# Optimization experiments

Measured on AMD Instinct MI355X. Metric: run time of the kernel, lower is better.

## Reference

```python
import jax, jax.numpy as jnp
import numpy as np

N = 8192      # nodes
E = 262144    # edges (avg degree 32)
NFEAT = 1024
NHID = 512
ZDIM = 32


def _uniform(key, shape, stdv):
    return jax.random.uniform(key, shape, jnp.float32, -stdv, stdv)


def setup_inputs() -> dict:
    key = jax.random.key(0)
    ks = jax.random.split(key, 10)
    x = jax.random.normal(ks[0], (N, NFEAT), jnp.float32)
    adj_rows = jnp.sort(jax.random.randint(ks[1], (E,), 0, N))
    adj_cols = jax.random.randint(ks[2], (E,), 0, N)
    # positive edge weights, roughly row-normalized (avg degree 32)
    adj_vals = jax.random.uniform(ks[3], (E,), jnp.float32) / 32.0
    s0 = 1.0 / np.sqrt(NHID).astype(np.float32)
    s1 = 1.0 / np.sqrt(ZDIM).astype(np.float32)
    W0 = _uniform(ks[4], (NFEAT, NHID), s0)
    b0 = _uniform(ks[5], (NHID,), s0)
    W1 = _uniform(ks[6], (NHID, ZDIM), s1)
    b1 = _uniform(ks[7], (ZDIM,), s1)
    W2 = _uniform(ks[8], (NHID, ZDIM), s1)
    b2 = _uniform(ks[9], (ZDIM,), s1)
    return dict(x=x, adj_vals=adj_vals, W0=W0, b0=b0, W1=W1, b1=b1,
                W2=W2, b2=b2, adj_rows=adj_rows, adj_cols=adj_cols)


def _spmm(rows, cols, vals, mat):
    # sparse [N,N] @ dense [N,D] via gather + segment_sum
    return jax.ops.segment_sum(vals[:, None] * mat[cols], rows, num_segments=N)


def reference(x, adj_vals, W0, b0, W1, b1, W2, b2, adj_rows, adj_cols):
    # GraphConvolution: spmm(adj, x @ W) + b  (eval mode: dropout is identity)
    h = jax.nn.relu(_spmm(adj_rows, adj_cols, adj_vals, x @ W0) + b0)
    mu = jax.nn.relu(_spmm(adj_rows, adj_cols, adj_vals, h @ W1) + b1)
    logvar = jax.nn.relu(_spmm(adj_rows, adj_cols, adj_vals, h @ W2) + b2)
    z = mu  # reparameterize in eval mode returns mu
    adj_recon = jax.nn.sigmoid(z @ z.T)  # [N, N] inner-product decoder
    return adj_recon, z, mu, logvar
```

## Files before the change

kernel.cpp:

```cpp
#include <hip/hip_runtime.h>
#include <hip/hip_bf16.h>

typedef __bf16 bf16_t;
typedef __bf16 bf16x8 __attribute__((ext_vector_type(8)));
typedef float f32x4 __attribute__((ext_vector_type(4)));

#define NN 8192
#define EE 262144
#define NF 1024
#define NH 512
#define ZD 32

__global__ __launch_bounds__(256) void k_cvt(const float* __restrict__ in,
                                             bf16_t* __restrict__ out, int n8) {
  int i = blockIdx.x * 256 + threadIdx.x;
  if (i >= n8) return;
  const float4 a = ((const float4*)in)[i * 2];
  const float4 b = ((const float4*)in)[i * 2 + 1];
  bf16x8 o;
  o[0] = (bf16_t)a.x; o[1] = (bf16_t)a.y; o[2] = (bf16_t)a.z; o[3] = (bf16_t)a.w;
  o[4] = (bf16_t)b.x; o[5] = (bf16_t)b.y; o[6] = (bf16_t)b.z; o[7] = (bf16_t)b.w;
  ((bf16x8*)out)[i] = o;
}

__global__ __launch_bounds__(256) void k_transpose_cvt(const float* __restrict__ in,
                                                       bf16_t* __restrict__ out,
                                                       int R, int C) {
  __shared__ float tile[32][33];
  const int c0 = blockIdx.x * 32, r0 = blockIdx.y * 32;
  const int tx = threadIdx.x & 31, ty = threadIdx.x >> 5;
  #pragma unroll
  for (int i = ty; i < 32; i += 8)
    tile[i][tx] = in[(size_t)(r0 + i) * C + (c0 + tx)];
  __syncthreads();
  #pragma unroll
  for (int i = ty; i < 32; i += 8)
    out[(size_t)(c0 + i) * R + (r0 + tx)] = (bf16_t)tile[tx][i];
}

__global__ __launch_bounds__(256) void k_transpose_w12(const float* __restrict__ W1,
                                                       const float* __restrict__ W2,
                                                       bf16_t* __restrict__ out) {
  __shared__ float tile[32][33];
  const float* in = blockIdx.z ? W2 : W1;
  bf16_t* o = out + (size_t)blockIdx.z * ZD * NH;
  const int r0 = blockIdx.y * 32;
  const int tx = threadIdx.x & 31, ty = threadIdx.x >> 5;
  #pragma unroll
  for (int i = ty; i < 32; i += 8)
    tile[i][tx] = in[(size_t)(r0 + i) * ZD + tx];
  __syncthreads();
  #pragma unroll
  for (int i = ty; i < 32; i += 8)
    o[(size_t)(i)*NH + (r0 + tx)] = (bf16_t)tile[tx][i];
}

__global__ void k_rowptr(const int* __restrict__ rows, int* __restrict__ rp,
                         int n, int e) {
  int r = blockIdx.x * 256 + threadIdx.x;
  if (r > n) return;
  if (r == n) { rp[n] = e; return; }
  int lo = 0, hi = e;
  while (lo < hi) { int mid = (lo + hi) >> 1; if (rows[mid] < r) lo = mid + 1; else hi = mid; }
  rp[r] = lo;
}

__global__ __launch_bounds__(256) void k_gemm_bt_128x128(
    const bf16_t* __restrict__ A, const bf16_t* __restrict__ Bt,
    bf16_t* __restrict__ C, int M, int N, int K) {
  __shared__ bf16_t As[128 * 32];
  __shared__ bf16_t Bs[128 * 32];
  const int tid = threadIdx.x;
  const int lane = tid & 63, wave = tid >> 6;
  const int wx = wave & 1, wy = wave >> 1;
  const int m0 = blockIdx.y * 128, n0 = blockIdx.x * 128;
  const int q = lane >> 4, ml = lane & 15;

  const int sr = tid >> 2, ss = tid & 3;
  const int sw_lo = sr * 32 + ((ss ^ (sr & 3)) * 8);
  const int sw_hi = sw_lo + 64 * 32;

  int a_off[4], b_off[4];
  #pragma unroll
  for (int i = 0; i < 4; ++i) {
    int m = wy * 64 + i * 16 + ml;
    a_off[i] = m * 32 + ((q ^ (m & 3)) * 8);
    int n = wx * 64 + i * 16 + ml;
    b_off[i] = n * 32 + ((q ^ (n & 3)) * 8);
  }

  f32x4 acc[4][4];
  #pragma unroll
  for (int i = 0; i < 4; ++i)
    #pragma unroll
    for (int j = 0; j < 4; ++j)
      acc[i][j] = (f32x4){0.f, 0.f, 0.f, 0.f};

  const bf16_t* ga = A + (size_t)(m0 + sr) * K + ss * 8;
  const bf16_t* gb = Bt + (size_t)(n0 + sr) * K + ss * 8;
  const size_t stride64 = (size_t)64 * K;

  for (int k0 = 0; k0 < K; k0 += 32) {
    int4 va0 = *(const int4*)(ga + k0);
    int4 va1 = *(const int4*)(ga + stride64 + k0);
    int4 vb0 = *(const int4*)(gb + k0);
    int4 vb1 = *(const int4*)(gb + stride64 + k0);
    __syncthreads();
    *(int4*)(&As[sw_lo]) = va0;
    *(int4*)(&As[sw_hi]) = va1;
    *(int4*)(&Bs[sw_lo]) = vb0;
    *(int4*)(&Bs[sw_hi]) = vb1;
    __syncthreads();
    bf16x8 af[4], bfr[4];
    #pragma unroll
    for (int i = 0; i < 4; ++i) af[i] = *(const bf16x8*)(&As[a_off[i]]);
    #pragma unroll
    for (int j = 0; j < 4; ++j) bfr[j] = *(const bf16x8*)(&Bs[b_off[j]]);
    #pragma unroll
    for (int i = 0; i < 4; ++i)
      #pragma unroll
      for (int j = 0; j < 4; ++j)
        acc[i][j] = __builtin_amdgcn_mfma_f32_16x16x32_bf16(af[i], bfr[j], acc[i][j], 0, 0, 0);
  }

  #pragma unroll
  for (int i = 0; i < 4; ++i) {
    const int row = m0 + wy * 64 + i * 16 + q * 4;
    #pragma unroll
    for (int j = 0; j < 4; ++j) {
      const int col = n0 + wx * 64 + j * 16 + ml;
      #pragma unroll
      for (int r = 0; r < 4; ++r)
        C[(size_t)(row + r) * N + col] = (bf16_t)acc[i][j][r];
    }
  }
}

__global__ __launch_bounds__(256) void k_gemm_bt_128x64(
    const bf16_t* __restrict__ A, const bf16_t* __restrict__ Bt,
    float* __restrict__ C, int M, int N, int K) {
  __shared__ bf16_t As[128 * 32];
  __shared__ bf16_t Bs[64 * 32];
  const int tid = threadIdx.x;
  const int lane = tid & 63, wave = tid >> 6;
  const int m0 = blockIdx.y * 128;
  const int q = lane >> 4, ml = lane & 15;
  const int sr = tid >> 2, ss = tid & 3;
  const int sw_lo = sr * 32 + ((ss ^ (sr & 3)) * 8);
  const int sw_hi = sw_lo + 64 * 32;

  int a_off[2], b_off[4];
  #pragma unroll
  for (int i = 0; i < 2; ++i) {
    int m = wave * 32 + i * 16 + ml;
    a_off[i] = m * 32 + ((q ^ (m & 3)) * 8);
  }
  #pragma unroll
  for (int j = 0; j < 4; ++j) {
    int n = j * 16 + ml;
    b_off[j] = n * 32 + ((q ^ (n & 3)) * 8);
  }

  f32x4 acc[2][4];
  #pragma unroll
  for (int i = 0; i < 2; ++i)
    #pragma unroll
    for (int j = 0; j < 4; ++j)
      acc[i][j] = (f32x4){0.f, 0.f, 0.f, 0.f};

  const bf16_t* ga = A + (size_t)(m0 + sr) * K + ss * 8;
  const bf16_t* gb = Bt + (size_t)sr * K + ss * 8;
  const size_t stride64 = (size_t)64 * K;

  for (int k0 = 0; k0 < K; k0 += 32) {
    int4 va0 = *(const int4*)(ga + k0);
    int4 va1 = *(const int4*)(ga + stride64 + k0);
    int4 vb0 = *(const int4*)(gb + k0);
    __syncthreads();
    *(int4*)(&As[sw_lo]) = va0;
    *(int4*)(&As[sw_hi]) = va1;
    *(int4*)(&Bs[sw_lo]) = vb0;
    __syncthreads();
    bf16x8 af[2], bfr[4];
    #pragma unroll
    for (int i = 0; i < 2; ++i) af[i] = *(const bf16x8*)(&As[a_off[i]]);
    #pragma unroll
    for (int j = 0; j < 4; ++j) bfr[j] = *(const bf16x8*)(&Bs[b_off[j]]);
    #pragma unroll
    for (int i = 0; i < 2; ++i)
      #pragma unroll
      for (int j = 0; j < 4; ++j)
        acc[i][j] = __builtin_amdgcn_mfma_f32_16x16x32_bf16(af[i], bfr[j], acc[i][j], 0, 0, 0);
  }

  #pragma unroll
  for (int i = 0; i < 2; ++i) {
    const int row = m0 + wave * 32 + i * 16 + q * 4;
    #pragma unroll
    for (int j = 0; j < 4; ++j) {
      const int col = j * 16 + ml;
      #pragma unroll
      for (int r = 0; r < 4; ++r)
        C[(size_t)(row + r) * N + col] = acc[i][j][r];
    }
  }
}

__global__ __launch_bounds__(256) void k_spmm_h(
    const int* __restrict__ rp, const int* __restrict__ cols,
    const float* __restrict__ vals, const unsigned int* __restrict__ XW0b,
    const float* __restrict__ b0, bf16_t* __restrict__ h) {
  const int chunk = blockIdx.x & 3;
  const int row = (blockIdx.x >> 2) * 4 + (threadIdx.x >> 6);
  const int t = threadIdx.x & 63;
  const unsigned int* tab = XW0b + chunk * 64 + t;
  int e = rp[row];
  const int end = rp[row + 1];
  float a0 = 0.f, a1 = 0.f;
  for (; e + 3 < end; e += 4) {
    const int c0 = cols[e], c1 = cols[e + 1], c2 = cols[e + 2], c3 = cols[e + 3];
    const float v0 = vals[e], v1 = vals[e + 1], v2 = vals[e + 2], v3 = vals[e + 3];
    const unsigned int p0 = tab[(size_t)c0 * 256];
    const unsigned int p1 = tab[(size_t)c1 * 256];
    const unsigned int p2 = tab[(size_t)c2 * 256];
    const unsigned int p3 = tab[(size_t)c3 * 256];
    a0 += v0 * __uint_as_float(p0 << 16);
    a1 += v0 * __uint_as_float(p0 & 0xffff0000u);
    a0 += v1 * __uint_as_float(p1 << 16);
    a1 += v1 * __uint_as_float(p1 & 0xffff0000u);
    a0 += v2 * __uint_as_float(p2 << 16);
    a1 += v2 * __uint_as_float(p2 & 0xffff0000u);
    a0 += v3 * __uint_as_float(p3 << 16);
    a1 += v3 * __uint_as_float(p3 & 0xffff0000u);
  }
  for (; e < end; ++e) {
    const float v0 = vals[e];
    const unsigned int p0 = tab[(size_t)cols[e] * 256];
    a0 += v0 * __uint_as_float(p0 << 16);
    a1 += v0 * __uint_as_float(p0 & 0xffff0000u);
  }
  const int d = chunk * 128 + t * 2;
  a0 += b0[d];
  a1 += b0[d + 1];
  bf16_t x0 = (bf16_t)fmaxf(a0, 0.f);
  bf16_t x1 = (bf16_t)fmaxf(a1, 0.f);
  const unsigned int pk = (unsigned int)(*(const unsigned short*)&x0) |
                          ((unsigned int)(*(const unsigned short*)&x1) << 16);
  *(unsigned int*)(h + (size_t)row * NH + d) = pk;
}

__global__ __launch_bounds__(256) void k_spmm_z(
    const int* __restrict__ rp, const int* __restrict__ cols,
    const float* __restrict__ vals, const float* __restrict__ HW,
    const float* __restrict__ b1, const float* __restrict__ b2,
    float* __restrict__ out_z, float* __restrict__ out_mu,
    float* __restrict__ out_lv, bf16_t* __restrict__ zb) {
  const int r = blockIdx.x * 4 + (threadIdx.x >> 6);
  const int t = threadIdx.x & 63;
  int e = rp[r];
  const int end = rp[r + 1];
  float acc = 0.f;
  for (; e + 3 < end; e += 4) {
    const float v0 = vals[e], v1 = vals[e + 1], v2 = vals[e + 2], v3 = vals[e + 3];
    const float s0 = HW[(size_t)cols[e] * 64 + t];
    const float s1 = HW[(size_t)cols[e + 1] * 64 + t];
    const float s2 = HW[(size_t)cols[e + 2] * 64 + t];
    const float s3 = HW[(size_t)cols[e + 3] * 64 + t];
    acc += v0 * s0;
    acc += v1 * s1;
    acc += v2 * s2;
    acc += v3 * s3;
  }
  for (; e < end; ++e) acc += vals[e] * HW[(size_t)cols[e] * 64 + t];
  const float b = (t < ZD) ? b1[t] : b2[t - ZD];
  const float v = fmaxf(acc + b, 0.f);
  if (t < ZD) {
    out_mu[(size_t)r * ZD + t] = v;
    out_z[(size_t)r * ZD + t] = v;
    zb[(size_t)r * ZD + t] = (bf16_t)v;
  } else {
    out_lv[(size_t)r * ZD + (t - ZD)] = v;
  }
}

__global__ __launch_bounds__(256) void k_decoder(const bf16_t* __restrict__ Z,
                                                 float* __restrict__ out) {
  __shared__ bf16_t Zr[128 * 32];
  __shared__ bf16_t Zc[128 * 32];
  __shared__ float tile[64][132];
  const int tid = threadIdx.x;
  const int lane = tid & 63, wave = tid >> 6;
  const int wx = wave & 1, wy = wave >> 1;
  const int m0 = blockIdx.y * 128, n0 = blockIdx.x * 128;
  const int q = lane >> 4, ml = lane & 15;
  const int sr = tid >> 2, ss = tid & 3;
  const int sw_lo = sr * 32 + ((ss ^ (sr & 3)) * 8);
  const int sw_hi = sw_lo + 64 * 32;

  *(int4*)(&Zr[sw_lo]) = *((const int4*)(Z + (size_t)(m0 + sr) * ZD) + ss);
  *(int4*)(&Zr[sw_hi]) = *((const int4*)(Z + (size_t)(m0 + sr + 64) * ZD) + ss);
  *(int4*)(&Zc[sw_lo]) = *((const int4*)(Z + (size_t)(n0 + sr) * ZD) + ss);
  *(int4*)(&Zc[sw_hi]) = *((const int4*)(Z + (size_t)(n0 + sr + 64) * ZD) + ss);
  __syncthreads();

  bf16x8 af[4], bfr[4];
  #pragma unroll
  for (int i = 0; i < 4; ++i) {
    int m = wy * 64 + i * 16 + ml;
    af[i] = *(const bf16x8*)(&Zr[m * 32 + ((q ^ (m & 3)) * 8)]);
    int n = wx * 64 + i * 16 + ml;
    bfr[i] = *(const bf16x8*)(&Zc[n * 32 + ((q ^ (n & 3)) * 8)]);
  }

  f32x4 acc[4][4];
  const f32x4 zero = (f32x4){0.f, 0.f, 0.f, 0.f};
  #pragma unroll
  for (int i = 0; i < 4; ++i)
    #pragma unroll
    for (int j = 0; j < 4; ++j)
      acc[i][j] = __builtin_amdgcn_mfma_f32_16x16x32_bf16(af[i], bfr[j], zero, 0, 0, 0);

  #pragma unroll
  for (int i = 0; i < 4; ++i)
    #pragma unroll
    for (int j = 0; j < 4; ++j)
      #pragma unroll
      for (int r = 0; r < 4; ++r)
        acc[i][j][r] = 1.f / (1.f + __expf(-acc[i][j][r]));

  const int g = tid >> 5, c4 = tid & 31;
  #pragma unroll
  for (int half = 0; half < 2; ++half) {
    if (wy == half) {
      #pragma unroll
      for (int i = 0; i < 4; ++i)
        #pragma unroll
        for (int j = 0; j < 4; ++j)
          #pragma unroll
          for (int r = 0; r < 4; ++r)
            tile[i * 16 + q * 4 + r][wx * 64 + j * 16 + ml] = acc[i][j][r];
    }
    __syncthreads();
    float* orow = out + (size_t)(m0 + half * 64) * NN + n0;
    #pragma unroll
    for (int p = 0; p < 8; ++p) {
      const int lr = p * 8 + g;
      f32x4 v = *(const f32x4*)&tile[lr][c4 * 4];
      __builtin_nontemporal_store(v, (f32x4*)(orow + (size_t)lr * NN + c4 * 4));
    }
    __syncthreads();
  }
}

extern "C" void kernel_launch(void* const* d_in, const int* in_sizes, int n_in,
                              void* d_out, int out_size, void* d_ws, size_t ws_size,
                              hipStream_t stream) {
  const float* x        = (const float*)d_in[0];
  const float* adj_vals = (const float*)d_in[1];
  const float* W0       = (const float*)d_in[2];
  const float* b0       = (const float*)d_in[3];
  const float* W1       = (const float*)d_in[4];
  const float* b1       = (const float*)d_in[5];
  const float* W2       = (const float*)d_in[6];
  const float* b2       = (const float*)d_in[7];
  const int* adj_rows   = (const int*)d_in[8];
  const int* adj_cols   = (const int*)d_in[9];

  char* ws = (char*)d_ws;
  bf16_t* XW0b = (bf16_t*)(ws);
  float*  HW   = (float*)(ws + 8388608);
  bf16_t* h    = (bf16_t*)(ws + 10485760);
  bf16_t* W0t  = (bf16_t*)(ws + 18874368);
  bf16_t* Wct  = (bf16_t*)(ws + 19922944);
  bf16_t* xb   = (bf16_t*)(ws + 19988480);
  bf16_t* zb   = (bf16_t*)(ws + 36765696);
  int*    rp   = (int*)(ws + 37289984);

  float* out     = (float*)d_out;
  float* out_adj = out;
  float* out_z   = out + (size_t)NN * NN;
  float* out_mu  = out_z + (size_t)NN * ZD;
  float* out_lv  = out_mu + (size_t)NN * ZD;

  k_cvt<<<(NN * NF / 8 + 255) / 256, 256, 0, stream>>>(x, xb, NN * NF / 8);
  k_transpose_cvt<<<dim3(NH / 32, NF / 32), 256, 0, stream>>>(W0, W0t, NF, NH);
  k_transpose_w12<<<dim3(1, NH / 32, 2), 256, 0, stream>>>(W1, W2, Wct);
  k_rowptr<<<33, 256, 0, stream>>>(adj_rows, rp, NN, EE);

  k_gemm_bt_128x128<<<dim3(NH / 128, NN / 128), 256, 0, stream>>>(xb, W0t, XW0b, NN, NH, NF);
  k_spmm_h<<<NN, 256, 0, stream>>>(rp, adj_cols, adj_vals,
                                   (const unsigned int*)XW0b, b0, h);

  k_gemm_bt_128x64<<<dim3(1, NN / 128), 256, 0, stream>>>(h, Wct, HW, NN, 64, NH);
  k_spmm_z<<<NN / 4, 256, 0, stream>>>(rp, adj_cols, adj_vals, HW, b1, b2, out_z, out_mu, out_lv, zb);

  k_decoder<<<dim3(NN / 128, NN / 128), 256, 0, stream>>>(zb, out_adj);
}
```

Baseline: 399.7 us.

## Fuse prep kernels, interleave edge data, stage edges in LDS for SpMM

Merges the four preprocessing launches into a single k_prep kernel that also packs cols/vals into an interleaved int2 edge array. Both SpMM kernels now load each 4-row group's edge list into shared memory once, instead of every wave re-reading cols/vals from global memory. k_spmm_h switches to 512-thread blocks with two chunks of four bf16 per lane (uint2 gathers), cutting block count and redundant edge reads. The aim is lower launch overhead and less edge-index traffic, at the cost of an extra pass writing the packed edge array and a global fallback path when a row group has more than 512 edges.

```diff
diff --git a/kernel.cpp b/kernel.cpp
--- a/kernel.cpp
+++ b/kernel.cpp
@@ -11,58 +11,70 @@
 #define NH 512
 #define ZD 32
 
-__global__ __launch_bounds__(256) void k_cvt(const float* __restrict__ in,
-                                             bf16_t* __restrict__ out, int n8) {
-  int i = blockIdx.x * 256 + threadIdx.x;
-  if (i >= n8) return;
-  const float4 a = ((const float4*)in)[i * 2];
-  const float4 b = ((const float4*)in)[i * 2 + 1];
-  bf16x8 o;
-  o[0] = (bf16_t)a.x; o[1] = (bf16_t)a.y; o[2] = (bf16_t)a.z; o[3] = (bf16_t)a.w;
-  o[4] = (bf16_t)b.x; o[5] = (bf16_t)b.y; o[6] = (bf16_t)b.z; o[7] = (bf16_t)b.w;
-  ((bf16x8*)out)[i] = o;
-}
-
-__global__ __launch_bounds__(256) void k_transpose_cvt(const float* __restrict__ in,
-                                                       bf16_t* __restrict__ out,
-                                                       int R, int C) {
+static __device__ __forceinline__ unsigned short bf16_bits(bf16_t v) {
+  union { bf16_t b; unsigned short u; } c;
+  c.b = v;
+  return c.u;
+}
+
+__global__ __launch_bounds__(256) void k_prep(
+    const float* __restrict__ x, bf16_t* __restrict__ xb,
+    const float* __restrict__ W0, bf16_t* __restrict__ W0t,
+    const float* __restrict__ W1, const float* __restrict__ W2, bf16_t* __restrict__ Wct,
+    const int* __restrict__ rows, int* __restrict__ rp,
+    const int* __restrict__ cols, const float* __restrict__ vals, int2* __restrict__ ev) {
   __shared__ float tile[32][33];
-  const int c0 = blockIdx.x * 32, r0 = blockIdx.y * 32;
-  const int tx = threadIdx.x & 31, ty = threadIdx.x >> 5;
-  #pragma unroll
-  for (int i = ty; i < 32; i += 8)
-    tile[i][tx] = in[(size_t)(r0 + i) * C + (c0 + tx)];
-  __syncthreads();
-  #pragma unroll
-  for (int i = ty; i < 32; i += 8)
-    out[(size_t)(c0 + i) * R + (r0 + tx)] = (bf16_t)tile[tx][i];
-}
-
-__global__ __launch_bounds__(256) void k_transpose_w12(const float* __restrict__ W1,
-                                                       const float* __restrict__ W2,
-                                                       bf16_t* __restrict__ out) {
-  __shared__ float tile[32][33];
-  const float* in = blockIdx.z ? W2 : W1;
-  bf16_t* o = out + (size_t)blockIdx.z * ZD * NH;
-  const int r0 = blockIdx.y * 32;
-  const int tx = threadIdx.x & 31, ty = threadIdx.x >> 5;
-  #pragma unroll
-  for (int i = ty; i < 32; i += 8)
-    tile[i][tx] = in[(size_t)(r0 + i) * ZD + tx];
-  __syncthreads();
-  #pragma unroll
-  for (int i = ty; i < 32; i += 8)
-    o[(size_t)(i)*NH + (r0 + tx)] = (bf16_t)tile[tx][i];
-}
-
-__global__ void k_rowptr(const int* __restrict__ rows, int* __restrict__ rp,
-                         int n, int e) {
-  int r = blockIdx.x * 256 + threadIdx.x;
-  if (r > n) return;
-  if (r == n) { rp[n] = e; return; }
-  int lo = 0, hi = e;
-  while (lo < hi) { int mid = (lo + hi) >> 1; if (rows[mid] < r) lo = mid + 1; else hi = mid; }
-  rp[r] = lo;
+  const int b = blockIdx.x;
+  const int tid = threadIdx.x;
+
+  if (b < 4096) {
+    const int i = b * 256 + tid;
+    const float4 a = ((const float4*)x)[i * 2];
+    const float4 c = ((const float4*)x)[i * 2 + 1];
+    bf16x8 o;
+    o[0] = (bf16_t)a.x; o[1] = (bf16_t)a.y; o[2] = (bf16_t)a.z; o[3] = (bf16_t)a.w;
+    o[4] = (bf16_t)c.x; o[5] = (bf16_t)c.y; o[6] = (bf16_t)c.z; o[7] = (bf16_t)c.w;
+    ((bf16x8*)xb)[i] = o;
+  } else if (b < 4608) {
+    const int bx = b - 4096;
+    const int c0 = (bx & 15) * 32, r0 = (bx >> 4) * 32;
+    const int tx = tid & 31, ty = tid >> 5;
+    #pragma unroll
+    for (int i = ty; i < 32; i += 8)
+      tile[i][tx] = W0[(size_t)(r0 + i) * NH + (c0 + tx)];
+    __syncthreads();
+    #pragma unroll
+    for (int i = ty; i < 32; i += 8)
+      W0t[(size_t)(c0 + i) * NF + (r0 + tx)] = (bf16_t)tile[tx][i];
+  } else if (b < 4640) {
+    const int idx = b - 4608;
+    const int z = idx & 1, y = idx >> 1;
+    const float* in = z ? W2 : W1;
+    bf16_t* o = Wct + (size_t)z * ZD * NH;
+    const int r0 = y * 32;
+    const int tx = tid & 31, ty = tid >> 5;
+    #pragma unroll
+    for (int i = ty; i < 32; i += 8)
+      tile[i][tx] = in[(size_t)(r0 + i) * ZD + tx];
+    __syncthreads();
+    #pragma unroll
+    for (int i = ty; i < 32; i += 8)
+      o[(size_t)(i)*NH + (r0 + tx)] = (bf16_t)tile[tx][i];
+  } else if (b < 4673) {
+    const int r = (b - 4640) * 256 + tid;
+    if (r > NN) return;
+    if (r == NN) { rp[NN] = EE; return; }
+    int lo = 0, hi = EE;
+    while (lo < hi) { int mid = (lo + hi) >> 1; if (rows[mid] < r) lo = mid + 1; else hi = mid; }
+    rp[r] = lo;
+  } else {
+    const int i = ((b - 4673) * 256 + tid) * 4;
+    const int4 c4 = *(const int4*)(cols + i);
+    const float4 v4 = *(const float4*)(vals + i);
+    int4* dst = (int4*)(ev + i);
+    dst[0] = make_int4(c4.x, __float_as_int(v4.x), c4.y, __float_as_int(v4.y));
+    dst[1] = make_int4(c4.z, __float_as_int(v4.z), c4.w, __float_as_int(v4.w));
+  }
 }
 
 __global__ __launch_bounds__(256) void k_gemm_bt_128x128(
@@ -206,72 +218,128 @@
   }
 }
 
-__global__ __launch_bounds__(256) void k_spmm_h(
-    const int* __restrict__ rp, const int* __restrict__ cols,
-    const float* __restrict__ vals, const unsigned int* __restrict__ XW0b,
-    const float* __restrict__ b0, bf16_t* __restrict__ h) {
-  const int chunk = blockIdx.x & 3;
-  const int row = (blockIdx.x >> 2) * 4 + (threadIdx.x >> 6);
-  const int t = threadIdx.x & 63;
-  const unsigned int* tab = XW0b + chunk * 64 + t;
-  int e = rp[row];
-  const int end = rp[row + 1];
-  float a0 = 0.f, a1 = 0.f;
-  for (; e + 3 < end; e += 4) {
-    const int c0 = cols[e], c1 = cols[e + 1], c2 = cols[e + 2], c3 = cols[e + 3];
-    const float v0 = vals[e], v1 = vals[e + 1], v2 = vals[e + 2], v3 = vals[e + 3];
-    const unsigned int p0 = tab[(size_t)c0 * 256];
-    const unsigned int p1 = tab[(size_t)c1 * 256];
-    const unsigned int p2 = tab[(size_t)c2 * 256];
-    const unsigned int p3 = tab[(size_t)c3 * 256];
-    a0 += v0 * __uint_as_float(p0 << 16);
-    a1 += v0 * __uint_as_float(p0 & 0xffff0000u);
-    a0 += v1 * __uint_as_float(p1 << 16);
-    a1 += v1 * __uint_as_float(p1 & 0xffff0000u);
-    a0 += v2 * __uint_as_float(p2 << 16);
-    a1 += v2 * __uint_as_float(p2 & 0xffff0000u);
-    a0 += v3 * __uint_as_float(p3 << 16);
-    a1 += v3 * __uint_as_float(p3 & 0xffff0000u);
+__global__ __launch_bounds__(512) void k_spmm_h(
+    const int* __restrict__ rp, const int2* __restrict__ ev,
+    const uint2* __restrict__ XW0b, const float* __restrict__ b0,
+    bf16_t* __restrict__ h) {
+  __shared__ int2 se[512];
+  const int rg = blockIdx.x;
+  const int tid = threadIdx.x;
+  const int wave = tid >> 6, t = tid & 63;
+  const int row = rg * 4 + (wave & 3);
+  const int chunk = wave >> 2;
+
+  const int base = rp[rg * 4];
+  const int cnt = rp[rg * 4 + 4] - base;
+  const int scnt = cnt < 512 ? cnt : 512;
+  for (int i = tid; i < scnt; i += 512) se[i] = ev[base + i];
+  __syncthreads();
+
+  int e = rp[row] - base;
+  const int end = rp[row + 1] - base;
+  const int se_end = end < 512 ? end : 512;
+  const uint2* tab = XW0b + chunk * 64 + t;
+
+  float a0 = 0.f, a1 = 0.f, a2 = 0.f, a3 = 0.f;
+  for (; e + 3 < se_end; e += 4) {
+    const int2 p0 = se[e], p1 = se[e + 1], p2 = se[e + 2], p3 = se[e + 3];
+    const uint2 g0 = tab[(size_t)p0.x * 128];
+    const uint2 g1 = tab[(size_t)p1.x * 128];
+    const uint2 g2 = tab[(size_t)p2.x * 128];
+    const uint2 g3 = tab[(size_t)p3.x * 128];
+    const float v0 = __int_as_float(p0.y), v1 = __int_as_float(p1.y);
+    const float v2 = __int_as_float(p2.y), v3 = __int_as_float(p3.y);
+    a0 += v0 * __uint_as_float(g0.x << 16);
+    a1 += v0 * __uint_as_float(g0.x & 0xffff0000u);
+    a2 += v0 * __uint_as_float(g0.y << 16);
+    a3 += v0 * __uint_as_float(g0.y & 0xffff0000u);
+    a0 += v1 * __uint_as_float(g1.x << 16);
+    a1 += v1 * __uint_as_float(g1.x & 0xffff0000u);
+    a2 += v1 * __uint_as_float(g1.y << 16);
+    a3 += v1 * __uint_as_float(g1.y & 0xffff0000u);
+    a0 += v2 * __uint_as_float(g2.x << 16);
+    a1 += v2 * __uint_as_float(g2.x & 0xffff0000u);
+    a2 += v2 * __uint_as_float(g2.y << 16);
+    a3 += v2 * __uint_as_float(g2.y & 0xffff0000u);
+    a0 += v3 * __uint_as_float(g3.x << 16);
+    a1 += v3 * __uint_as_float(g3.x & 0xffff0000u);
+    a2 += v3 * __uint_as_float(g3.y << 16);
+    a3 += v3 * __uint_as_float(g3.y & 0xffff0000u);
+  }
+  for (; e < se_end; ++e) {
+    const int2 p = se[e];
+    const uint2 g = tab[(size_t)p.x * 128];
+    const float v = __int_as_float(p.y);
+    a0 += v * __uint_as_float(g.x << 16);
+    a1 += v * __uint_as_float(g.x & 0xffff0000u);
+    a2 += v * __uint_as_float(g.y << 16);
+    a3 += v * __uint_as_float(g.y & 0xffff0000u);
   }
   for (; e < end; ++e) {
-    const float v0 = vals[e];
-    const unsigned int p0 = tab[(size_t)cols[e] * 256];
-    a0 += v0 * __uint_as_float(p0 << 16);
-    a1 += v0 * __uint_as_float(p0 & 0xffff0000u);
-  }
-  const int d = chunk * 128 + t * 2;
-  a0 += b0[d];
-  a1 += b0[d + 1];
-  bf16_t x0 = (bf16_t)fmaxf(a0, 0.f);
-  bf16_t x1 = (bf16_t)fmaxf(a1, 0.f);
-  const unsigned int pk = (unsigned int)(*(const unsigned short*)&x0) |
-                          ((unsigned int)(*(const unsigned short*)&x1) << 16);
-  *(unsigned int*)(h + (size_t)row * NH + d) = pk;
+    const int2 p = ev[base + e];
+    const uint2 g = tab[(size_t)p.x * 128];
+    const float v = __int_as_float(p.y);
+    a0 += v * __uint_as_float(g.x << 16);
+    a1 += v * __uint_as_float(g.x & 0xffff0000u);
+    a2 += v * __uint_as_float(g.y << 16);
+    a3 += v * __uint_as_float(g.y & 0xffff0000u);
+  }
+
+  const int d = chunk * 256 + t * 4;
+  const float4 bb = *(const float4*)(b0 + d);
+  const bf16_t x0 = (bf16_t)fmaxf(a0 + bb.x, 0.f);
+  const bf16_t x1 = (bf16_t)fmaxf(a1 + bb.y, 0.f);
+  const bf16_t x2 = (bf16_t)fmaxf(a2 + bb.z, 0.f);
+  const bf16_t x3 = (bf16_t)fmaxf(a3 + bb.w, 0.f);
+  uint2 pk;
+  pk.x = (unsigned int)bf16_bits(x0) | ((unsigned int)bf16_bits(x1) << 16);
+  pk.y = (unsigned int)bf16_bits(x2) | ((unsigned int)bf16_bits(x3) << 16);
+  ((uint2*)(h + (size_t)row * NH))[chunk * 64 + t] = pk;
 }
 
 __global__ __launch_bounds__(256) void k_spmm_z(
-    const int* __restrict__ rp, const int* __restrict__ cols,
-    const float* __restrict__ vals, const float* __restrict__ HW,
+    const int* __restrict__ rp, const int2* __restrict__ ev,
+    const float* __restrict__ HW,
     const float* __restrict__ b1, const float* __restrict__ b2,
     float* __restrict__ out_z, float* __restrict__ out_mu,
     float* __restrict__ out_lv, bf16_t* __restrict__ zb) {
-  const int r = blockIdx.x * 4 + (threadIdx.x >> 6);
-  const int t = threadIdx.x & 63;
-  int e = rp[r];
-  const int end = rp[r + 1];
+  __shared__ int2 se[512];
+  const int rg = blockIdx.x;
+  const int tid = threadIdx.x;
+  const int r = rg * 4 + (tid >> 6);
+  const int t = tid & 63;
+
+  const int base = rp[rg * 4];
+  const int cnt = rp[rg * 4 + 4] - base;
+  const int scnt = cnt < 512 ? cnt : 512;
+  for (int i = tid; i < scnt; i += 256) se[i] = ev[base + i];
+  __syncthreads();
+
+  int e = rp[r] - base;
+  const int end = rp[r + 1] - base;
+  const int se_end = end < 512 ? end : 512;
+
   float acc = 0.f;
-  for (; e + 3 < end; e += 4) {
-    const float v0 = vals[e], v1 = vals[e + 1], v2 = vals[e + 2], v3 = vals[e + 3];
-    const float s0 = HW[(size_t)cols[e] * 64 + t];
-    const float s1 = HW[(size_t)cols[e + 1] * 64 + t];
-    const float s2 = HW[(size_t)cols[e + 2] * 64 + t];
-    const float s3 = HW[(size_t)cols[e + 3] * 64 + t];
-    acc += v0 * s0;
-    acc += v1 * s1;
-    acc += v2 * s2;
-    acc += v3 * s3;
-  }
-  for (; e < end; ++e) acc += vals[e] * HW[(size_t)cols[e] * 64 + t];
+  for (; e + 3 < se_end; e += 4) {
+    const int2 p0 = se[e], p1 = se[e + 1], p2 = se[e + 2], p3 = se[e + 3];
+    const float s0 = HW[(size_t)p0.x * 64 + t];
+    const float s1 = HW[(size_t)p1.x * 64 + t];
+    const float s2 = HW[(size_t)p2.x * 64 + t];
+    const float s3 = HW[(size_t)p3.x * 64 + t];
+    acc += __int_as_float(p0.y) * s0;
+    acc += __int_as_float(p1.y) * s1;
+    acc += __int_as_float(p2.y) * s2;
+    acc += __int_as_float(p3.y) * s3;
+  }
+  for (; e < se_end; ++e) {
+    const int2 p = se[e];
+    acc += __int_as_float(p.y) * HW[(size_t)p.x * 64 + t];
+  }
+  for (; e < end; ++e) {
+    const int2 p = ev[base + e];
+    acc += __int_as_float(p.y) * HW[(size_t)p.x * 64 + t];
+  }
+
   const float b = (t < ZD) ? b1[t] : b2[t - ZD];
   const float v = fmaxf(acc + b, 0.f);
   if (t < ZD) {
@@ -375,6 +443,7 @@
   bf16_t* xb   = (bf16_t*)(ws + 19988480);
   bf16_t* zb   = (bf16_t*)(ws + 36765696);
   int*    rp   = (int*)(ws + 37289984);
+  int2*   ev   = (int2*)(ws + 37322768);
 
   float* out     = (float*)d_out;
   float* out_adj = out;
@@ -382,17 +451,14 @@
   float* out_mu  = out_z + (size_t)NN * ZD;
   float* out_lv  = out_mu + (size_t)NN * ZD;
 
-  k_cvt<<<(NN * NF / 8 + 255) / 256, 256, 0, stream>>>(x, xb, NN * NF / 8);
-  k_transpose_cvt<<<dim3(NH / 32, NF / 32), 256, 0, stream>>>(W0, W0t, NF, NH);
-  k_transpose_w12<<<dim3(1, NH / 32, 2), 256, 0, stream>>>(W1, W2, Wct);
-  k_rowptr<<<33, 256, 0, stream>>>(adj_rows, rp, NN, EE);
+  k_prep<<<4929, 256, 0, stream>>>(x, xb, W0, W0t, W1, W2, Wct,
+                                   adj_rows, rp, adj_cols, adj_vals, ev);
 
   k_gemm_bt_128x128<<<dim3(NH / 128, NN / 128), 256, 0, stream>>>(xb, W0t, XW0b, NN, NH, NF);
-  k_spmm_h<<<NN, 256, 0, stream>>>(rp, adj_cols, adj_vals,
-                                   (const unsigned int*)XW0b, b0, h);
+  k_spmm_h<<<NN / 4, 512, 0, stream>>>(rp, ev, (const uint2*)XW0b, b0, h);
 
   k_gemm_bt_128x64<<<dim3(1, NN / 128), 256, 0, stream>>>(h, Wct, HW, NN, 64, NH);
-  k_spmm_z<<<NN / 4, 256, 0, stream>>>(rp, adj_cols, adj_vals, HW, b1, b2, out_z, out_mu, out_lv, zb);
+  k_spmm_z<<<NN / 4, 256, 0, stream>>>(rp, ev, HW, b1, b2, out_z, out_mu, out_lv, zb);
 
   k_decoder<<<dim3(NN / 128, NN / 128), 256, 0, stream>>>(zb, out_adj);
 }
```

Measured after the change: 379.8 us. 1.05x faster.
